# Performance work log

Hardware: AMD Instinct MI355X
Metric: run time of the kernel (lower is better)

## Reference

```python
import jax, jax.numpy as jnp
import numpy as np

HEADS = 4
HEAD_DIM = 32  # hidden_dim // num_heads = 128 // 4
HIDDEN = 128
NEG_SLOPE = 0.2  # GATConv default


def gat_conv(x, src, dst, W, att_src, att_dst, bias):
    """PyG GATConv (concat=True, default negative_slope=0.2), eval mode.
    x: [N, F_in], src/dst: [E] (self-loops already included)."""
    N = x.shape[0]
    h = (x @ W).reshape(N, HEADS, HEAD_DIM)               # [N, H, D]
    a_src = jnp.einsum('nhd,hd->nh', h, att_src)          # [N, H]
    a_dst = jnp.einsum('nhd,hd->nh', h, att_dst)
    e = jax.nn.leaky_relu(a_src[src] + a_dst[dst], NEG_SLOPE)  # [E, H]
    # numerically stable softmax over incoming edges of each dst node
    m = jax.ops.segment_max(e, dst, num_segments=N)
    m = jnp.where(jnp.isfinite(m), m, 0.0)
    p = jnp.exp(e - m[dst])
    denom = jax.ops.segment_sum(p, dst, num_segments=N)
    alpha = p / (denom[dst] + 1e-16)                      # [E, H]
    out = jax.ops.segment_sum(h[src] * alpha[..., None], dst, num_segments=N)
    return out.reshape(N, HEADS * HEAD_DIM) + bias


def setup_inputs() -> dict:
    key = jax.random.key(0)
    ks = jax.random.split(key, 20)
    n_news, n_tweets, E = 20000, 80000, 1600000
    N = n_news + n_tweets
    s = 0.05
    inp = {
        'x_news': jax.random.normal(ks[0], (n_news, 768), jnp.float32),
        'x_tweets': jax.random.normal(ks[1], (n_tweets, 512), jnp.float32),
        'edge_index': jax.random.randint(ks[2], (2, E), 0, N, jnp.int32),
        'W_news': jax.random.normal(ks[3], (768, HIDDEN), jnp.float32) * s,
        'b_news': jnp.zeros((HIDDEN,), jnp.float32),
        'W_tw': jax.random.normal(ks[4], (512, HIDDEN), jnp.float32) * s,
        'b_tw': jnp.zeros((HIDDEN,), jnp.float32),
        'gat1_W': jax.random.normal(ks[5], (HIDDEN, HIDDEN), jnp.float32) * s,
        'gat1_as': jax.random.normal(ks[6], (HEADS, HEAD_DIM), jnp.float32) * s,
        'gat1_ad': jax.random.normal(ks[7], (HEADS, HEAD_DIM), jnp.float32) * s,
        'gat1_b': jnp.zeros((HIDDEN,), jnp.float32),
        'gat2_W': jax.random.normal(ks[8], (HIDDEN, HIDDEN), jnp.float32) * s,
        'gat2_as': jax.random.normal(ks[9], (HEADS, HEAD_DIM), jnp.float32) * s,
        'gat2_ad': jax.random.normal(ks[10], (HEADS, HEAD_DIM), jnp.float32) * s,
        'gat2_b': jnp.zeros((HIDDEN,), jnp.float32),
        'Wc1': jax.random.normal(ks[11], (HIDDEN, HIDDEN // 2), jnp.float32) * s,
        'bc1': jnp.zeros((HIDDEN // 2,), jnp.float32),
        'Wc2': jax.random.normal(ks[12], (HIDDEN // 2, 2), jnp.float32) * s,
        'bc2': jnp.zeros((2,), jnp.float32),
    }
    return inp


def reference(x_news, x_tweets, edge_index, W_news, b_news, W_tw, b_tw,
              gat1_W, gat1_as, gat1_ad, gat1_b,
              gat2_W, gat2_as, gat2_ad, gat2_b,
              Wc1, bc1, Wc2, bc2):
    n_news = x_news.shape[0]
    # encoders (dropout is identity in eval)
    h_news = jax.nn.relu(x_news @ W_news + b_news)
    h_tw = jax.nn.relu(x_tweets @ W_tw + b_tw)
    x = jnp.concatenate([h_news, h_tw], axis=0)           # [N, 128]
    N = x.shape[0]
    # GATConv default: add self-loops
    loops = jnp.arange(N, dtype=edge_index.dtype)
    src = jnp.concatenate([edge_index[0], loops])
    dst = jnp.concatenate([edge_index[1], loops])
    x = jax.nn.elu(gat_conv(x, src, dst, gat1_W, gat1_as, gat1_ad, gat1_b))
    x = jax.nn.elu(gat_conv(x, src, dst, gat2_W, gat2_as, gat2_ad, gat2_b))
    news_emb = x[:n_news]
    out = jax.nn.relu(news_emb @ Wc1 + bc1) @ Wc2 + bc2   # [n_news, 2]
    return out
```

## Files before the change

kernel.cpp:

```cpp
#include <hip/hip_runtime.h>
#include <hip/hip_bf16.h>
#include <type_traits>

typedef __attribute__((ext_vector_type(8))) short bf16x8;
typedef __attribute__((ext_vector_type(8))) unsigned short u16x8;
typedef __attribute__((ext_vector_type(4))) float f32x4;

__device__ __forceinline__ unsigned short f2b(float f) {
  union { float f; unsigned u; } c; c.f = f;
  return (unsigned short)((c.u + 0x7fffu + ((c.u >> 16) & 1u)) >> 16);
}
__device__ __forceinline__ float b2f(unsigned short v) {
  return __uint_as_float((unsigned)v << 16);
}

constexpr int BK = 64;
constexpr int LS = BK + 8;

template<int BM, int K, int ACT, int LOGITS, typename AT>
__device__ __forceinline__ void gemm_body(
    int bid, unsigned short* As, unsigned short* Bs,
    const AT* __restrict__ A, int M,
    const unsigned short* __restrict__ WT, const float* __restrict__ bias,
    unsigned short* __restrict__ C,
    const float* __restrict__ att_src, const float* __restrict__ att_dst,
    float* __restrict__ a_src, float* __restrict__ a_dst)
{
  constexpr int WR = (BM >= 128) ? 2 : 1;
  constexpr int WC = 4 / WR;
  constexpr int WTM = BM / WR;
  constexpr int WTN = 128 / WC;
  constexpr int MF = WTM / 16;
  constexpr int NF = WTN / 16;
  constexpr int HPW = NF / 2;
  const int t = threadIdx.x;
  const int lane = t & 63;
  const int wave = t >> 6;
  const int wr = wave / WC, wc = wave % WC;
  const long row0 = (long)bid * BM;

  f32x4 acc[MF][NF] = {};

  for (int k0 = 0; k0 < K; k0 += BK) {
    if constexpr (std::is_same<AT, float>::value) {
#pragma unroll
      for (int i = 0; i < BM / 16; ++i) {
        int idx = t + i * 256;
        int r = idx >> 4;
        int kq = idx & 15;
        long gr = row0 + r; if (gr >= M) gr = M - 1;
        const float4 v = *(const float4*)(A + gr * K + k0 + kq * 4);
        ushort4 b;
        b.x = f2b(v.x); b.y = f2b(v.y); b.z = f2b(v.z); b.w = f2b(v.w);
        *(ushort4*)(&As[r * LS + kq * 4]) = b;
      }
    } else {
#pragma unroll
      for (int i = 0; i < BM / 32; ++i) {
        int idx = t + i * 256;
        int r = idx >> 3;
        int k8 = idx & 7;
        long gr = row0 + r; if (gr >= M) gr = M - 1;
        u16x8 v = *(const u16x8*)(A + gr * K + k0 + k8 * 8);
        *(u16x8*)(&As[r * LS + k8 * 8]) = v;
      }
    }
#pragma unroll
    for (int i = 0; i < 4; ++i) {
      int idx = t + i * 256;
      int col = idx >> 3;
      int k8 = idx & 7;
      u16x8 v = *(const u16x8*)(WT + (long)col * K + k0 + k8 * 8);
      *(u16x8*)(&Bs[col * LS + k8 * 8]) = v;
    }
    __syncthreads();
#pragma unroll
    for (int kk = 0; kk < BK; kk += 32) {
      const int koff = kk + (lane >> 4) * 8;
      bf16x8 af[MF], bfr[NF];
#pragma unroll
      for (int m = 0; m < MF; ++m)
        af[m] = *(const bf16x8*)(&As[(wr * WTM + m * 16 + (lane & 15)) * LS + koff]);
#pragma unroll
      for (int n = 0; n < NF; ++n)
        bfr[n] = *(const bf16x8*)(&Bs[(wc * WTN + n * 16 + (lane & 15)) * LS + koff]);
#pragma unroll
      for (int m = 0; m < MF; ++m)
#pragma unroll
        for (int n = 0; n < NF; ++n)
          acc[m][n] = __builtin_amdgcn_mfma_f32_16x16x32_bf16(af[m], bfr[n], acc[m][n], 0, 0, 0);
    }
    __syncthreads();
  }

  float asv[NF], adv[NF];
  if (LOGITS) {
#pragma unroll
    for (int n = 0; n < NF; ++n) {
      int hd = wc * HPW + (n >> 1);
      int dim = (n & 1) * 16 + (lane & 15);
      asv[n] = att_src[hd * 32 + dim];
      adv[n] = att_dst[hd * 32 + dim];
    }
  }

#pragma unroll
  for (int m = 0; m < MF; ++m) {
#pragma unroll
    for (int j = 0; j < 4; ++j) {
      long gr = row0 + wr * WTM + m * 16 + (lane >> 4) * 4 + j;
      if (gr < M) {
#pragma unroll
        for (int n = 0; n < NF; ++n) {
          int c = wc * WTN + n * 16 + (lane & 15);
          float v = acc[m][n][j];
          if (bias) v += bias[c];
          if (ACT == 1) v = fmaxf(v, 0.f);
          C[gr * 128 + c] = f2b(v);
        }
      }
      if (LOGITS) {
        float sa[HPW], da[HPW];
#pragma unroll
        for (int g = 0; g < HPW; ++g) {
          sa[g] = fmaf(acc[m][2 * g][j], asv[2 * g], acc[m][2 * g + 1][j] * asv[2 * g + 1]);
          da[g] = fmaf(acc[m][2 * g][j], adv[2 * g], acc[m][2 * g + 1][j] * adv[2 * g + 1]);
        }
#pragma unroll
        for (int off = 1; off < 16; off <<= 1) {
#pragma unroll
          for (int g = 0; g < HPW; ++g) {
            sa[g] += __shfl_xor(sa[g], off);
            da[g] += __shfl_xor(da[g], off);
          }
        }
        if ((lane & 15) == 0 && gr < M) {
#pragma unroll
          for (int g = 0; g < HPW; ++g) {
            a_src[gr * 4 + wc * HPW + g] = sa[g];
            a_dst[gr * 4 + wc * HPW + g] = da[g];
          }
        }
      }
    }
  }
}

__device__ __forceinline__ void hist_body(int bid, int* cnt, const int* __restrict__ dst,
                                          int E, int* __restrict__ bcount, int nb)
{
  int t = threadIdx.x;
  for (int b = t; b < 512; b += 256) cnt[b] = 0;
  __syncthreads();
  int e0 = bid * 8192;
  for (int i = 0; i < 32; ++i) {
    int e = e0 + i * 256 + t;
    if (e < E) atomicAdd(&cnt[dst[e] >> 8], 1);
  }
  __syncthreads();
  for (int b = t; b < nb; b += 256) {
    int c = cnt[b];
    if (c > 0) atomicAdd(&bcount[b], c);
  }
}

__device__ __forceinline__ void scatter_body(int bid, int* s, const int* __restrict__ src,
                                             const int* __restrict__ dst, int E,
                                             int* __restrict__ bcur, int2* __restrict__ pairs)
{
  int* cnt = s;
  int* base = s + 512;
  int* rcur = s + 1024;
  int t = threadIdx.x;
  for (int b = t; b < 512; b += 256) { cnt[b] = 0; rcur[b] = 0; }
  __syncthreads();
  int e0 = bid * 8192;
  for (int i = 0; i < 32; ++i) {
    int e = e0 + i * 256 + t;
    if (e < E) atomicAdd(&cnt[dst[e] >> 8], 1);
  }
  __syncthreads();
  for (int b = t; b < 512; b += 256) {
    int c = cnt[b];
    if (c > 0) base[b] = atomicAdd(&bcur[b], c);
  }
  __syncthreads();
  for (int i = 0; i < 32; ++i) {
    int e = e0 + i * 256 + t;
    if (e < E) {
      int d = dst[e];
      int b = d >> 8;
      int off = atomicAdd(&rcur[b], 1);
      int2 p; p.x = src[e]; p.y = d;
      pairs[base[b] + off] = p;
    }
  }
}

__global__ __launch_bounds__(256) void mega1_kernel(
    int nb_tw, int nb_news,
    const float* __restrict__ x_tw, int n_tw, const unsigned short* __restrict__ WT_tw,
    const float* __restrict__ b_tw, unsigned short* __restrict__ out_tw,
    const float* __restrict__ x_news, int n_news, const unsigned short* __restrict__ WT_news,
    const float* __restrict__ b_news, unsigned short* __restrict__ out_news,
    const int* __restrict__ dst, int E, int* __restrict__ bcount, int nb)
{
  __shared__ unsigned short sh[(64 + 128) * LS];
  int bid = blockIdx.x;
  if (bid < nb_tw) {
    gemm_body<64, 512, 1, 0, float>(bid, sh, sh + 64 * LS, x_tw, n_tw, WT_tw, b_tw, out_tw,
                                    nullptr, nullptr, nullptr, nullptr);
  } else if (bid < nb_tw + nb_news) {
    gemm_body<32, 768, 1, 0, float>(bid - nb_tw, sh, sh + 32 * LS, x_news, n_news, WT_news,
                                    b_news, out_news, nullptr, nullptr, nullptr, nullptr);
  } else {
    hist_body(bid - nb_tw - nb_news, (int*)sh, dst, E, bcount, nb);
  }
}

__global__ __launch_bounds__(256) void mega3_kernel(
    int nb_gemm,
    const unsigned short* __restrict__ x_feat, int N, const unsigned short* __restrict__ WT_g1,
    unsigned short* __restrict__ h_feat,
    const float* __restrict__ g1as, const float* __restrict__ g1ad,
    float* __restrict__ a_src, float* __restrict__ a_dst,
    const int* __restrict__ src, const int* __restrict__ dst, int E,
    int* __restrict__ bcur, int2* __restrict__ pairs)
{
  __shared__ unsigned short sh[(64 + 128) * LS];
  int bid = blockIdx.x;
  if (bid < nb_gemm) {
    gemm_body<64, 128, 0, 1, unsigned short>(bid, sh, sh + 64 * LS, x_feat, N, WT_g1, nullptr,
                                             h_feat, g1as, g1ad, a_src, a_dst);
  } else {
    scatter_body(bid - nb_gemm, (int*)sh, src, dst, E, bcur, pairs);
  }
}

template<int BM, int K, int ACT, int LOGITS, typename AT>
__global__ __launch_bounds__(256) void gemm_kernel(
    const AT* __restrict__ A, int M,
    const unsigned short* __restrict__ WT, const float* __restrict__ bias,
    unsigned short* __restrict__ C,
    const float* __restrict__ att_src, const float* __restrict__ att_dst,
    float* __restrict__ a_src, float* __restrict__ a_dst)
{
  __shared__ unsigned short sh[(BM + 128) * LS];
  gemm_body<BM, K, ACT, LOGITS, AT>(blockIdx.x, sh, sh + BM * LS, A, M, WT, bias, C,
                                    att_src, att_dst, a_src, a_dst);
}

__global__ void transpose_all_kernel(const float* __restrict__ W0, unsigned short* __restrict__ T0,
                                     const float* __restrict__ W1, unsigned short* __restrict__ T1,
                                     const float* __restrict__ W2, unsigned short* __restrict__ T2,
                                     const float* __restrict__ W3, unsigned short* __restrict__ T3)
{
  int r = blockIdx.x * 256 + threadIdx.x;
  if (r < 128 * 768) { int c = r / 768, k = r - c * 768; T0[r] = f2b(W0[(size_t)k * 128 + c]); return; }
  r -= 128 * 768;
  if (r < 128 * 512) { int c = r / 512, k = r - c * 512; T1[r] = f2b(W1[(size_t)k * 128 + c]); return; }
  r -= 128 * 512;
  if (r < 128 * 128) { T2[r] = f2b(W2[(size_t)(r & 127) * 128 + (r >> 7)]); return; }
  r -= 128 * 128;
  if (r < 128 * 128) { T3[r] = f2b(W3[(size_t)(r & 127) * 128 + (r >> 7)]); return; }
}

__global__ __launch_bounds__(512) void bucket_scan_kernel(const int* __restrict__ bcount, int nb, int E,
                                                          int* __restrict__ bstart, int* __restrict__ bcur,
                                                          int* __restrict__ row_ptr, int N)
{
  __shared__ int s[512];
  int t = threadIdx.x;
  int my = (t < nb) ? bcount[t] : 0;
  s[t] = my;
  __syncthreads();
  for (int off = 1; off < 512; off <<= 1) {
    int v = (t >= off) ? s[t - off] : 0;
    __syncthreads();
    s[t] += v;
    __syncthreads();
  }
  int excl = s[t] - my;
  if (t < nb) { bstart[t] = excl; bcur[t] = excl; }
  if (t == 0) { bstart[nb] = E; row_ptr[N] = E; }
}

__global__ __launch_bounds__(256) void bucket_csr_kernel(const int2* __restrict__ pairs,
                                                         const int* __restrict__ bstart, int N,
                                                         int* __restrict__ row_ptr, int* __restrict__ col_idx)
{
  __shared__ int cnt[256];
  __shared__ int excl[256];
  __shared__ int cur[256];
  int t = threadIdx.x;
  int nodebase = blockIdx.x << 8;
  int start = bstart[blockIdx.x];
  int size = bstart[blockIdx.x + 1] - start;
  cnt[t] = 0;
  __syncthreads();
  for (int i = t; i < size; i += 256)
    atomicAdd(&cnt[pairs[start + i].y & 255], 1);
  __syncthreads();
  int my = cnt[t];
  excl[t] = my;
  __syncthreads();
  for (int off = 1; off < 256; off <<= 1) {
    int v = (t >= off) ? excl[t - off] : 0;
    __syncthreads();
    excl[t] += v;
    __syncthreads();
  }
  int ex = excl[t] - my;
  if (nodebase + t < N) row_ptr[nodebase + t] = start + ex;
  excl[t] = ex;
  cur[t] = 0;
  __syncthreads();
  for (int i = t; i < size; i += 256) {
    int2 p = pairs[start + i];
    int local = p.y & 255;
    int pos = start + excl[local] + atomicAdd(&cur[local], 1);
    col_idx[pos] = p.x;
  }
}

__global__ void gat_aggregate_kernel(const unsigned short* __restrict__ h, const float* __restrict__ a_src,
                                     const float* __restrict__ a_dst, const int* __restrict__ row_ptr,
                                     const int* __restrict__ col_idx, const float* __restrict__ bias,
                                     int N, unsigned short* __restrict__ out)
{
  int n = (blockIdx.x * blockDim.x + threadIdx.x) >> 6;
  int lane = threadIdx.x & 63;
  if (n >= N) return;
  const int sub = lane >> 4;
  const int sl = lane & 15;
  const int head = sl >> 2;
  const int beg = row_ptr[n], end = row_ptr[n + 1];
  const float adst = a_dst[(size_t)n * 4 + head];

  float slf = a_src[(size_t)n * 4 + head] + adst;
  slf = fmaxf(slf, 0.2f * slf);
  float ps = (sub == 0) ? __expf(slf) : 0.f;
  float denom = ps;
  float acc[8];
  {
    const u16x8 hs = *(const u16x8*)(h + (size_t)n * 128 + 8 * sl);
#pragma unroll
    for (int j = 0; j < 8; ++j) acc[j] = ps * b2f(hs[j]);
  }

  int e = beg + sub;
  for (; e + 4 < end; e += 8) {
    const int s0 = col_idx[e];
    const int s1 = col_idx[e + 4];
    const u16x8 h0 = *(const u16x8*)(h + (size_t)s0 * 128 + 8 * sl);
    const u16x8 h1 = *(const u16x8*)(h + (size_t)s1 * 128 + 8 * sl);
    float l0 = a_src[(size_t)s0 * 4 + head] + adst;
    float l1 = a_src[(size_t)s1 * 4 + head] + adst;
    l0 = fmaxf(l0, 0.2f * l0);
    l1 = fmaxf(l1, 0.2f * l1);
    const float p0 = __expf(l0);
    const float p1 = __expf(l1);
    denom += p0 + p1;
#pragma unroll
    for (int j = 0; j < 8; ++j) {
      acc[j] = fmaf(p0, b2f(h0[j]), acc[j]);
      acc[j] = fmaf(p1, b2f(h1[j]), acc[j]);
    }
  }
  if (e < end) {
    const int s = col_idx[e];
    const u16x8 hv = *(const u16x8*)(h + (size_t)s * 128 + 8 * sl);
    float lg = a_src[(size_t)s * 4 + head] + adst;
    lg = fmaxf(lg, 0.2f * lg);
    const float p = __expf(lg);
    denom += p;
#pragma unroll
    for (int j = 0; j < 8; ++j) acc[j] = fmaf(p, b2f(hv[j]), acc[j]);
  }

#pragma unroll
  for (int j = 0; j < 8; ++j) {
    acc[j] += __shfl_xor(acc[j], 16);
    acc[j] += __shfl_xor(acc[j], 32);
  }
  denom += __shfl_xor(denom, 16);
  denom += __shfl_xor(denom, 32);

  if (sub == 0) {
    const float inv = 1.0f / (denom + 1e-16f);
    const float4 b0 = *(const float4*)(bias + 8 * sl);
    const float4 b1 = *(const float4*)(bias + 8 * sl + 4);
    float o[8];
    o[0] = acc[0] * inv + b0.x; o[1] = acc[1] * inv + b0.y;
    o[2] = acc[2] * inv + b0.z; o[3] = acc[3] * inv + b0.w;
    o[4] = acc[4] * inv + b1.x; o[5] = acc[5] * inv + b1.y;
    o[6] = acc[6] * inv + b1.z; o[7] = acc[7] * inv + b1.w;
    u16x8 r;
#pragma unroll
    for (int j = 0; j < 8; ++j) {
      float v = (o[j] > 0.f) ? o[j] : expm1f(o[j]);
      r[j] = f2b(v);
    }
    *(u16x8*)(out + (size_t)n * 128 + 8 * sl) = r;
  }
}

__global__ void classifier_kernel(const unsigned short* __restrict__ x, const float* __restrict__ Wc1,
                                  const float* __restrict__ bc1, const float* __restrict__ Wc2,
                                  const float* __restrict__ bc2, float* __restrict__ out, int M)
{
  int row = (blockIdx.x * blockDim.x + threadIdx.x) >> 6;
  int lane = threadIdx.x & 63;
  if (row >= M) return;
  const unsigned short* xr = x + (size_t)row * 128;
  float c = 0.f;
#pragma unroll 8
  for (int k = 0; k < 128; k += 2) {
    unsigned v = *(const unsigned*)(xr + k);
    c = fmaf(__uint_as_float(v << 16), Wc1[k * 64 + lane], c);
    c = fmaf(__uint_as_float(v & 0xffff0000u), Wc1[(k + 1) * 64 + lane], c);
  }
  c += bc1[lane];
  c = fmaxf(c, 0.f);
  float o0 = c * Wc2[lane * 2 + 0];
  float o1 = c * Wc2[lane * 2 + 1];
#pragma unroll
  for (int off = 1; off < 64; off <<= 1) {
    o0 += __shfl_xor(o0, off);
    o1 += __shfl_xor(o1, off);
  }
  if (lane == 0) {
    out[(size_t)row * 2 + 0] = o0 + bc2[0];
    out[(size_t)row * 2 + 1] = o1 + bc2[1];
  }
}

extern "C" void kernel_launch(void* const* d_in, const int* in_sizes, int n_in,
                              void* d_out, int out_size, void* d_ws, size_t ws_size,
                              hipStream_t stream)
{
  const float* x_news = (const float*)d_in[0];
  const float* x_tw   = (const float*)d_in[1];
  const int*   ei     = (const int*)d_in[2];
  const float* W_news = (const float*)d_in[3];
  const float* b_news = (const float*)d_in[4];
  const float* W_tw   = (const float*)d_in[5];
  const float* b_tw   = (const float*)d_in[6];
  const float* g1W  = (const float*)d_in[7];
  const float* g1as = (const float*)d_in[8];
  const float* g1ad = (const float*)d_in[9];
  const float* g1b  = (const float*)d_in[10];
  const float* g2W  = (const float*)d_in[11];
  const float* g2as = (const float*)d_in[12];
  const float* g2ad = (const float*)d_in[13];
  const float* g2b  = (const float*)d_in[14];
  const float* Wc1  = (const float*)d_in[15];
  const float* bc1  = (const float*)d_in[16];
  const float* Wc2  = (const float*)d_in[17];
  const float* bc2  = (const float*)d_in[18];

  const int n_news = in_sizes[0] / 768;
  const int n_tw   = in_sizes[1] / 512;
  const int N = n_news + n_tw;
  const int E = in_sizes[2] / 2;
  const int* src = ei;
  const int* dst = ei + E;
  const int nb = (N + 255) >> 8;

  char* ws = (char*)d_ws;
  size_t off = 0;
  auto alloc = [&](size_t bytes) -> void* {
    void* p = ws + off;
    off += (bytes + 255) & ~(size_t)255;
    return p;
  };
  unsigned short* x_feat = (unsigned short*)alloc((size_t)N * 128 * 2);
  unsigned short* h_feat = (unsigned short*)alloc((size_t)N * 128 * 2);
  float* a_src   = (float*)alloc((size_t)N * 4 * 4);
  float* a_dst   = (float*)alloc((size_t)N * 4 * 4);
  int*   row_ptr = (int*)alloc((size_t)(N + 1) * 4);
  int*   col_idx = (int*)alloc((size_t)E * 4);
  int2*  pairs   = (int2*)alloc((size_t)E * 8);
  int*   bcount  = (int*)alloc(2048);
  int*   bstart  = (int*)alloc(2052);
  int*   bcur    = (int*)alloc(2048);
  unsigned short* WT_news = (unsigned short*)alloc((size_t)128 * 768 * 2);
  unsigned short* WT_tw   = (unsigned short*)alloc((size_t)128 * 512 * 2);
  unsigned short* WT_g1   = (unsigned short*)alloc((size_t)128 * 128 * 2);
  unsigned short* WT_g2   = (unsigned short*)alloc((size_t)128 * 128 * 2);

  hipMemsetAsync(bcount, 0, 2048, stream);

  transpose_all_kernel<<<768, 256, 0, stream>>>(W_news, WT_news, W_tw, WT_tw, g1W, WT_g1, g2W, WT_g2);

  const int nb_tw = (n_tw + 63) / 64;
  const int nb_news = (n_news + 31) / 32;
  const int nb_hist = (E + 8191) / 8192;
  mega1_kernel<<<nb_tw + nb_news + nb_hist, 256, 0, stream>>>(
      nb_tw, nb_news,
      x_tw, n_tw, WT_tw, b_tw, x_feat + (size_t)n_news * 128,
      x_news, n_news, WT_news, b_news, x_feat,
      dst, E, bcount, nb);

  bucket_scan_kernel<<<1, 512, 0, stream>>>(bcount, nb, E, bstart, bcur, row_ptr, N);

  const int nb_g = (N + 63) / 64;
  mega3_kernel<<<nb_g + nb_hist, 256, 0, stream>>>(
      nb_g, x_feat, N, WT_g1, h_feat, g1as, g1ad, a_src, a_dst,
      src, dst, E, bcur, pairs);

  bucket_csr_kernel<<<nb, 256, 0, stream>>>(pairs, bstart, N, row_ptr, col_idx);

  gat_aggregate_kernel<<<(N + 3) / 4, 256, 0, stream>>>(h_feat, a_src, a_dst, row_ptr, col_idx, g1b, N, x_feat);

  gemm_kernel<64, 128, 0, 1, unsigned short><<<nb_g, 256, 0, stream>>>(
      x_feat, N, WT_g2, nullptr, h_feat, g2as, g2ad, a_src, a_dst);
  gat_aggregate_kernel<<<(N + 3) / 4, 256, 0, stream>>>(h_feat, a_src, a_dst, row_ptr, col_idx, g2b, N, x_feat);

  classifier_kernel<<<(n_news + 3) / 4, 256, 0, stream>>>(x_feat, Wc1, bc1, Wc2, bc2, (float*)d_out, n_news);
}
```

Baseline: 367.9 us.

## Load GEMM weight fragments directly from global memory instead of LDS staging

The weight tile is no longer staged in shared memory. Each wave reads its bf16 B fragments straight from global, and the warp layout is fixed to one wave per 32-column head slice. This cuts the LDS footprint to the A tile only, which may raise occupancy, and removes the B copy and its share of the barrier work. In exchange, B reads now go through L1/L2 with less coalesced per-lane accesses, and waves that share rows no longer share those loads. BM=128 configurations lose the 2-row wave split and now run MF=8 per wave.

```diff
diff --git a/kernel.cpp b/kernel.cpp
--- a/kernel.cpp
+++ b/kernel.cpp
@@ -19,24 +19,21 @@
 
 template<int BM, int K, int ACT, int LOGITS, typename AT>
 __device__ __forceinline__ void gemm_body(
-    int bid, unsigned short* As, unsigned short* Bs,
+    int bid, unsigned short* As,
     const AT* __restrict__ A, int M,
     const unsigned short* __restrict__ WT, const float* __restrict__ bias,
     unsigned short* __restrict__ C,
     const float* __restrict__ att_src, const float* __restrict__ att_dst,
     float* __restrict__ a_src, float* __restrict__ a_dst)
 {
-  constexpr int WR = (BM >= 128) ? 2 : 1;
-  constexpr int WC = 4 / WR;
-  constexpr int WTM = BM / WR;
-  constexpr int WTN = 128 / WC;
+  constexpr int WTM = BM;
+  constexpr int WTN = 32;
   constexpr int MF = WTM / 16;
   constexpr int NF = WTN / 16;
-  constexpr int HPW = NF / 2;
+  constexpr int HPW = 1;
   const int t = threadIdx.x;
   const int lane = t & 63;
-  const int wave = t >> 6;
-  const int wr = wave / WC, wc = wave % WC;
+  const int wc = t >> 6;
   const long row0 = (long)bid * BM;
 
   f32x4 acc[MF][NF] = {};
@@ -65,25 +62,17 @@
         *(u16x8*)(&As[r * LS + k8 * 8]) = v;
       }
     }
-#pragma unroll
-    for (int i = 0; i < 4; ++i) {
-      int idx = t + i * 256;
-      int col = idx >> 3;
-      int k8 = idx & 7;
-      u16x8 v = *(const u16x8*)(WT + (long)col * K + k0 + k8 * 8);
-      *(u16x8*)(&Bs[col * LS + k8 * 8]) = v;
-    }
     __syncthreads();
 #pragma unroll
     for (int kk = 0; kk < BK; kk += 32) {
       const int koff = kk + (lane >> 4) * 8;
       bf16x8 af[MF], bfr[NF];
 #pragma unroll
+      for (int n = 0; n < NF; ++n)
+        bfr[n] = *(const bf16x8*)(WT + (long)(wc * WTN + n * 16 + (lane & 15)) * K + k0 + koff);
+#pragma unroll
       for (int m = 0; m < MF; ++m)
-        af[m] = *(const bf16x8*)(&As[(wr * WTM + m * 16 + (lane & 15)) * LS + koff]);
-#pragma unroll
-      for (int n = 0; n < NF; ++n)
-        bfr[n] = *(const bf16x8*)(&Bs[(wc * WTN + n * 16 + (lane & 15)) * LS + koff]);
+        af[m] = *(const bf16x8*)(&As[(m * 16 + (lane & 15)) * LS + koff]);
 #pragma unroll
       for (int m = 0; m < MF; ++m)
 #pragma unroll
@@ -97,10 +86,9 @@
   if (LOGITS) {
 #pragma unroll
     for (int n = 0; n < NF; ++n) {
-      int hd = wc * HPW + (n >> 1);
-      int dim = (n & 1) * 16 + (lane & 15);
-      asv[n] = att_src[hd * 32 + dim];
-      adv[n] = att_dst[hd * 32 + dim];
+      int dim = n * 16 + (lane & 15);
+      asv[n] = att_src[wc * 32 + dim];
+      adv[n] = att_dst[wc * 32 + dim];
     }
   }
 
@@ -108,7 +96,7 @@
   for (int m = 0; m < MF; ++m) {
 #pragma unroll
     for (int j = 0; j < 4; ++j) {
-      long gr = row0 + wr * WTM + m * 16 + (lane >> 4) * 4 + j;
+      long gr = row0 + m * 16 + (lane >> 4) * 4 + j;
       if (gr < M) {
 #pragma unroll
         for (int n = 0; n < NF; ++n) {
@@ -120,26 +108,16 @@
         }
       }
       if (LOGITS) {
-        float sa[HPW], da[HPW];
-#pragma unroll
-        for (int g = 0; g < HPW; ++g) {
-          sa[g] = fmaf(acc[m][2 * g][j], asv[2 * g], acc[m][2 * g + 1][j] * asv[2 * g + 1]);
-          da[g] = fmaf(acc[m][2 * g][j], adv[2 * g], acc[m][2 * g + 1][j] * adv[2 * g + 1]);
-        }
+        float sa = fmaf(acc[m][0][j], asv[0], acc[m][1][j] * asv[1]);
+        float da = fmaf(acc[m][0][j], adv[0], acc[m][1][j] * adv[1]);
 #pragma unroll
         for (int off = 1; off < 16; off <<= 1) {
-#pragma unroll
-          for (int g = 0; g < HPW; ++g) {
-            sa[g] += __shfl_xor(sa[g], off);
-            da[g] += __shfl_xor(da[g], off);
-          }
+          sa += __shfl_xor(sa, off);
+          da += __shfl_xor(da, off);
         }
         if ((lane & 15) == 0 && gr < M) {
-#pragma unroll
-          for (int g = 0; g < HPW; ++g) {
-            a_src[gr * 4 + wc * HPW + g] = sa[g];
-            a_dst[gr * 4 + wc * HPW + g] = da[g];
-          }
+          a_src[gr * 4 + wc] = sa;
+          a_dst[gr * 4 + wc] = da;
         }
       }
     }
@@ -205,13 +183,13 @@
     const float* __restrict__ b_news, unsigned short* __restrict__ out_news,
     const int* __restrict__ dst, int E, int* __restrict__ bcount, int nb)
 {
-  __shared__ unsigned short sh[(64 + 128) * LS];
+  __shared__ unsigned short sh[64 * LS];
   int bid = blockIdx.x;
   if (bid < nb_tw) {
-    gemm_body<64, 512, 1, 0, float>(bid, sh, sh + 64 * LS, x_tw, n_tw, WT_tw, b_tw, out_tw,
+    gemm_body<64, 512, 1, 0, float>(bid, sh, x_tw, n_tw, WT_tw, b_tw, out_tw,
                                     nullptr, nullptr, nullptr, nullptr);
   } else if (bid < nb_tw + nb_news) {
-    gemm_body<32, 768, 1, 0, float>(bid - nb_tw, sh, sh + 32 * LS, x_news, n_news, WT_news,
+    gemm_body<32, 768, 1, 0, float>(bid - nb_tw, sh, x_news, n_news, WT_news,
                                     b_news, out_news, nullptr, nullptr, nullptr, nullptr);
   } else {
     hist_body(bid - nb_tw - nb_news, (int*)sh, dst, E, bcount, nb);
@@ -227,10 +205,10 @@
     const int* __restrict__ src, const int* __restrict__ dst, int E,
     int* __restrict__ bcur, int2* __restrict__ pairs)
 {
-  __shared__ unsigned short sh[(64 + 128) * LS];
+  __shared__ unsigned short sh[64 * LS];
   int bid = blockIdx.x;
   if (bid < nb_gemm) {
-    gemm_body<64, 128, 0, 1, unsigned short>(bid, sh, sh + 64 * LS, x_feat, N, WT_g1, nullptr,
+    gemm_body<64, 128, 0, 1, unsigned short>(bid, sh, x_feat, N, WT_g1, nullptr,
                                              h_feat, g1as, g1ad, a_src, a_dst);
   } else {
     scatter_body(bid - nb_gemm, (int*)sh, src, dst, E, bcur, pairs);
@@ -245,8 +223,8 @@
     const float* __restrict__ att_src, const float* __restrict__ att_dst,
     float* __restrict__ a_src, float* __restrict__ a_dst)
 {
-  __shared__ unsigned short sh[(BM + 128) * LS];
-  gemm_body<BM, K, ACT, LOGITS, AT>(blockIdx.x, sh, sh + BM * LS, A, M, WT, bias, C,
+  __shared__ unsigned short sh[BM * LS];
+  gemm_body<BM, K, ACT, LOGITS, AT>(blockIdx.x, sh, A, M, WT, bias, C,
                                     att_src, att_dst, a_src, a_dst);
 }
 
```

Result: no change. 375.0 us (+1.9%).
